# Kernel tuning notes

Measured on AMD Instinct MI355X. Metric: run time of the kernel, lower is better.

Reference implementation:

```python
import jax, jax.numpy as jnp
import numpy as np
import math

NUM_HEADS = 16  # power of two -> simple ALiBi slope formula

def alibi_slopes(num_heads: int) -> jnp.ndarray:
    # num_heads is a power of two here; general formula per Press et al. 2022
    k = 1 << (num_heads.bit_length() - 1)
    ratio = 2.0 ** (-8.0 / k)
    slopes = ratio ** np.arange(1, 1 + k)
    if num_heads != k:
        ratio2 = 2.0 ** (-8.0 / (2 * k))
        rest = (ratio2 ** np.arange(1, 1 + 2 * k, 2))[: num_heads - k]
        slopes = np.concatenate([slopes, rest])
    return jnp.asarray(slopes, dtype=jnp.float32).reshape(1, -1, 1, 1)


def setup_inputs() -> dict:
    key = jax.random.key(0)
    kq, kk, kv, km = jax.random.split(key, 4)
    B, H, S, D = 1, NUM_HEADS, 2048, 64
    query = jax.random.normal(kq, (B, H, S, D), dtype=jnp.float32)
    k_ = jax.random.normal(kk, (B, H, S, D), dtype=jnp.float32)
    value = jax.random.normal(kv, (B, H, S, D), dtype=jnp.float32)
    # padding-style boolean mask [B, S]; keep position 0 always valid
    mask = jax.random.randint(km, (B, S), 0, 2).astype(bool)
    mask = mask.at[:, 0].set(True)
    return {"query": query, "key": k_, "value": value, "mask": mask}


def reference(query, key, value, mask):
    B, H, S, D = query.shape
    scale = 1.0 / math.sqrt(D)
    # scores: [B, H, Sq, Sk]
    scores = jnp.einsum("bhqd,bhkd->bhqk", query, key) * scale
    # causal ALiBi bias: distances arange(1-S, 1) -> shape (1, H, 1, S)
    distances = jnp.arange(1 - S, 1, dtype=jnp.float32)
    bias = distances[None, None, None, :] * alibi_slopes(H)
    scores = scores + bias
    # boolean padding mask [B, S] -> [B, 1, 1, S]
    blocked = jnp.finfo(scores.dtype).min
    scores = jnp.where(mask[:, None, None, :], scores, blocked)
    weights = jax.nn.softmax(scores, axis=-1)
    # dropout_prob = 0.0 (eval) -> identity
    return jnp.einsum("bhqk,bhkd->bhqd", weights, value)
```

## Files before the change

kernel.cpp:

```cpp
#include <hip/hip_runtime.h>


constexpr int   S_LEN  = 2048;
constexpr int   D_DIM  = 64;
constexpr int   H_NUM  = 16;
constexpr int   QT     = 128;
constexpr int   K_TILE = 64;
constexpr int   NTILE  = S_LEN / K_TILE;
constexpr int   MAXNC  = 8;
constexpr int   QB     = S_LEN / QT;
constexpr int   HC0    = 6;
constexpr int   PROWSTR= 36;
constexpr float SCL    = 0.18033688f;
constexpr float L2E    = 1.44269504f;
constexpr float MASKED = -50000.0f;
constexpr float CUTOFF = 40.0f;

typedef short bf16x8 __attribute__((ext_vector_type(8)));
typedef short bf16x4 __attribute__((ext_vector_type(4)));
typedef float f32x4  __attribute__((ext_vector_type(4)));

__device__ inline short f2bf(float f) {
    union { float f; unsigned u; } x; x.f = f;
    return (short)((x.u + 0x7fffu + ((x.u >> 16) & 1u)) >> 16);
}

__device__ inline unsigned pack2bf(float a, float b) {
#if __has_builtin(__builtin_amdgcn_cvt_pk_bf16_f32)
    auto p = __builtin_amdgcn_cvt_pk_bf16_f32(a, b);
    unsigned u; __builtin_memcpy(&u, &p, 4); return u;
#else
    return (unsigned)(unsigned short)f2bf(a) | ((unsigned)(unsigned short)f2bf(b) << 16);
#endif
}

__device__ inline float fexp2(float x) {
#if __has_builtin(__builtin_amdgcn_exp2f)
    return __builtin_amdgcn_exp2f(x);
#else
    return exp2f(x);
#endif
}

__device__ inline unsigned permb(unsigned hi, unsigned lo, unsigned sel) {
#if __has_builtin(__builtin_amdgcn_perm)
    return __builtin_amdgcn_perm(hi, lo, sel);
#else
    return (sel == 0x05040100u) ? ((lo & 0xffffu) | (hi << 16))
                                : ((lo >> 16) | (hi & 0xffff0000u));
#endif
}

__device__ inline void load_lds16(const void* g, void* l) {
    __builtin_amdgcn_global_load_lds((const __attribute__((address_space(1))) void*)g,
                                     (__attribute__((address_space(3))) void*)l, 16, 0, 0);
}

__device__ inline int head_t0(int h) {
    const float slope_l2e = exp2f(-0.5f * (float)(h + 1)) * L2E;
    const float kmin = 2047.0f - CUTOFF / slope_l2e;
    return kmin <= 0.0f ? 0 : ((int)kmin) >> 6;
}
__device__ inline int head_nc(int h) {
    const int nt = NTILE - head_t0(h);
    const int nc = (nt + 3) >> 2;
    return nc > MAXNC ? MAXNC : nc;
}

__global__ __launch_bounds__(256)
void preprocess_kernel(const float* __restrict__ Qm, const float* __restrict__ Km,
                       const float* __restrict__ Vm, const void* __restrict__ maskp,
                       short* __restrict__ Qbf, short* __restrict__ Kswz,
                       short* __restrict__ Vswz, float* __restrict__ Bias)
{
    __shared__ int mask_is_i32;
    const int tid = threadIdx.x;
    const int kt = blockIdx.x, h = blockIdx.y;

    {
        const int row = kt * 64 + (tid >> 2);
        const int col = (tid & 3) << 4;
        const float* src = Qm + ((size_t)h * S_LEN + row) * D_DIM + col;
        short* dst = Qbf + ((size_t)h * S_LEN + row) * D_DIM + col;
        #pragma unroll
        for (int j = 0; j < 2; ++j) {
            float4 a = *(const float4*)(src + j * 8);
            float4 b = *(const float4*)(src + j * 8 + 4);
            unsigned u[4] = { pack2bf(a.x * SCL, a.y * SCL), pack2bf(a.z * SCL, a.w * SCL),
                              pack2bf(b.x * SCL, b.y * SCL), pack2bf(b.z * SCL, b.w * SCL) };
            bf16x8 qp; __builtin_memcpy(&qp, u, 16);
            *(bf16x8*)(dst + j * 8) = qp;
        }
    }

    if (kt < head_t0(h)) return;

    const int kbase = kt * K_TILE;
    const size_t tbase = ((size_t)h * S_LEN + kbase) * D_DIM;
    short* Kd = Kswz + ((size_t)h * NTILE + kt) * 4096;
    short* Vd = Vswz + ((size_t)h * NTILE + kt) * 4096;

    if (tid < 64) {
        const unsigned v = ((const unsigned*)maskp)[tid];
        const unsigned long long b = __ballot(v <= 1u);
        if (tid == 0) mask_is_i32 = (b == ~0ULL);
    }

    #pragma unroll
    for (int it = 0; it < 2; ++it) {
        const int idx = it * 256 + tid;
        const int key = idx >> 3, c = idx & 7;
        const float* src = Km + tbase + key * 64 + c * 8;
        float4 a = *(const float4*)src;
        float4 b = *(const float4*)(src + 4);
        unsigned u[4] = { pack2bf(a.x, a.y), pack2bf(a.z, a.w),
                          pack2bf(b.x, b.y), pack2bf(b.z, b.w) };
        bf16x8 kp; __builtin_memcpy(&kp, u, 16);
        *(bf16x8*)(Kd + key * 64 + ((c ^ (key & 7)) << 3)) = kp;
    }

    {
        const int db = tid >> 4, kb = tid & 15;
        const int d4 = db * 4, key4 = kb * 4;
        float4 vv[4];
        #pragma unroll
        for (int j = 0; j < 4; ++j)
            vv[j] = *(const float4*)(Vm + tbase + (key4 + j) * 64 + d4);
        const float* vp = (const float*)vv;
        #pragma unroll
        for (int jj = 0; jj < 4; ++jj) {
            const int d = d4 + jj;
            bf16x4 ov;
            ov[0] = f2bf(vp[0 * 4 + jj]); ov[1] = f2bf(vp[1 * 4 + jj]);
            ov[2] = f2bf(vp[2 * 4 + jj]); ov[3] = f2bf(vp[3 * 4 + jj]);
            *(bf16x4*)(Vd + d * 64 + (((key4 >> 3) ^ (d & 7)) << 3) + (key4 & 7)) = ov;
        }
    }
    __syncthreads();
    if (tid < K_TILE) {
        const int key = kbase + tid;
        const int mv = mask_is_i32 ? ((const int*)maskp)[key]
                                   : (int)((const unsigned char*)maskp)[key];
        const float slope_l2e = exp2f(-0.5f * (float)(h + 1)) * L2E;
        Bias[h * S_LEN + key] = mv ? slope_l2e * (float)(key - (S_LEN - 1)) : MASKED;
    }
}

__global__ __launch_bounds__(256, 4)
void attn_main(const short* __restrict__ Qbf, const short* __restrict__ Kswz,
               const short* __restrict__ Vswz, const float* __restrict__ Bias,
               float* __restrict__ Om, unsigned* __restrict__ Opart,
               float* __restrict__ lp)
{
    __shared__ short    k_lds[4096];
    __shared__ short    v_lds[4096];
    __shared__ float    bm_lds[64];
    __shared__ unsigned p_lds[4][32 * PROWSTR];

    const int tid = threadIdx.x;
    const int wave = tid >> 6, lane = tid & 63;
    const int l16 = lane & 15, quad = lane >> 4;
    const int h = blockIdx.y, qblk = blockIdx.x, c = blockIdx.z;

    const int nc = head_nc(h);
    if (c >= nc) return;
    const int t0 = head_t0(h);
    const int nt = NTILE - t0;
    const int tstart = t0 + (c * nt) / nc;
    const int tend   = t0 + ((c + 1) * nt) / nc;

    const unsigned psel = (quad < 2) ? 0x05040100u : 0x07060302u;

    bf16x8 qfrag[2][2];
    {
        const short* Qh = Qbf + (size_t)h * S_LEN * D_DIM;
        #pragma unroll
        for (int s = 0; s < 2; ++s) {
            const int qrow = qblk * QT + wave * 32 + s * 16 + l16;
            #pragma unroll
            for (int t = 0; t < 2; ++t)
                qfrag[s][t] = *(const bf16x8*)(Qh + (size_t)qrow * D_DIM + t * 32 + quad * 8);
        }
    }

    bf16x8 onesv;
    #pragma unroll
    for (int i = 0; i < 8; ++i) onesv[i] = (short)0x3F80;

    f32x4 o_frag[2][4], l4[2];
    #pragma unroll
    for (int s = 0; s < 2; ++s) {
        #pragma unroll
        for (int cc = 0; cc < 4; ++cc) o_frag[s][cc] = (f32x4){0.f, 0.f, 0.f, 0.f};
        l4[s] = (f32x4){0.f, 0.f, 0.f, 0.f};
    }

    const short* Kh = Kswz + (size_t)h * NTILE * 4096;
    const short* Vh = Vswz + (size_t)h * NTILE * 4096;
    const float* Bh = Bias + h * S_LEN;
    unsigned* pw = p_lds[wave];
    const int swz = l16 & 7;

    for (int kt = tstart; kt < tend; ++kt) {
        __syncthreads();
        {
            const char* kg = (const char*)(Kh + (size_t)kt * 4096);
            const char* vg = (const char*)(Vh + (size_t)kt * 4096);
            char* kl = (char*)k_lds + wave * 2048;
            char* vl = (char*)v_lds + wave * 2048;
            const int go = wave * 2048 + lane * 16;
            load_lds16(kg + go,        kl);
            load_lds16(kg + go + 1024, kl + 1024);
            load_lds16(vg + go,        vl);
            load_lds16(vg + go + 1024, vl + 1024);
        }
        if (tid < 16) {
            float4 b4 = *(const float4*)(Bh + kt * K_TILE + tid * 4);
            *(float4*)&bm_lds[tid * 4] = b4;
        }
        __syncthreads();

        f32x4 sv[2][4];
        #pragma unroll
        for (int cc = 0; cc < 4; ++cc) {
            const float b = bm_lds[cc * 16 + l16];
            const f32x4 binit = (f32x4){b, b, b, b};
            sv[0][cc] = binit;
            sv[1][cc] = binit;
            #pragma unroll
            for (int t = 0; t < 2; ++t) {
                bf16x8 bfrag = *(const bf16x8*)&k_lds[(cc * 16 + l16) * 64 + (((t * 4 + quad) ^ swz) << 3)];
                sv[0][cc] = __builtin_amdgcn_mfma_f32_16x16x32_bf16(qfrag[0][t], bfrag, sv[0][cc], 0, 0, 0);
                sv[1][cc] = __builtin_amdgcn_mfma_f32_16x16x32_bf16(qfrag[1][t], bfrag, sv[1][cc], 0, 0, 0);
            }
        }

        #pragma unroll
        for (int s = 0; s < 2; ++s) {
            #pragma unroll
            for (int r = 0; r < 4; ++r) {
                const float p0 = fexp2(sv[s][0][r]);
                const float p1 = fexp2(sv[s][1][r]);
                const float p2 = fexp2(sv[s][2][r]);
                const float p3 = fexp2(sv[s][3][r]);
                unsigned* pp = &pw[(s * 16 + quad * 4 + r) * PROWSTR + l16];
                pp[0]  = pack2bf(p0, p1);
                pp[16] = pack2bf(p2, p3);
            }
        }

        #pragma unroll
        for (int t2 = 0; t2 < 2; ++t2) {
            bf16x8 pfrag[2];
            #pragma unroll
            for (int s = 0; s < 2; ++s) {
                const unsigned* pr = &pw[(s * 16 + l16) * PROWSTR + t2 * 16 + (quad & 1) * 8];
                uint4 w0 = *(const uint4*)(pr);
                uint4 w1 = *(const uint4*)(pr + 4);
                unsigned pf[4];
                pf[0] = permb(w0.y, w0.x, psel);
                pf[1] = permb(w0.w, w0.z, psel);
                pf[2] = permb(w1.y, w1.x, psel);
                pf[3] = permb(w1.w, w1.z, psel);
                __builtin_memcpy(&pfrag[s], pf, 16);
            }
            #pragma unroll
            for (int c2 = 0; c2 < 4; ++c2) {
                bf16x8 vfrag = *(const bf16x8*)&v_lds[(c2 * 16 + l16) * 64 + (((t2 * 4 + quad) ^ swz) << 3)];
                o_frag[0][c2] = __builtin_amdgcn_mfma_f32_16x16x32_bf16(pfrag[0], vfrag, o_frag[0][c2], 0, 0, 0);
                o_frag[1][c2] = __builtin_amdgcn_mfma_f32_16x16x32_bf16(pfrag[1], vfrag, o_frag[1][c2], 0, 0, 0);
            }
            l4[0] = __builtin_amdgcn_mfma_f32_16x16x32_bf16(pfrag[0], onesv, l4[0], 0, 0, 0);
            l4[1] = __builtin_amdgcn_mfma_f32_16x16x32_bf16(pfrag[1], onesv, l4[1], 0, 0, 0);
        }
    }

    if (nc == 1) {
        float* Oh = Om + (size_t)h * S_LEN * D_DIM;
        const int qrow0 = qblk * QT + wave * 32;
        #pragma unroll
        for (int s = 0; s < 2; ++s) {
            #pragma unroll
            for (int r = 0; r < 4; ++r) {
                const float inv = 1.0f / l4[s][r];
                const int row = qrow0 + s * 16 + quad * 4 + r;
                float* dst = Oh + (size_t)row * D_DIM + l16;
                dst[0]  = o_frag[s][0][r] * inv;
                dst[16] = o_frag[s][1][r] * inv;
                dst[32] = o_frag[s][2][r] * inv;
                dst[48] = o_frag[s][3][r] * inv;
            }
        }
        return;
    }

    #pragma unroll
    for (int s = 0; s < 2; ++s) {
        const int g = qblk * 32 + wave * 8 + s * 4 + quad;
        const size_t gbase = (((size_t)h * MAXNC + c) * 512 + g);
        #pragma unroll
        for (int c2 = 0; c2 < 4; ++c2) {
            uint2 pk;
            pk.x = pack2bf(o_frag[s][c2][0], o_frag[s][c2][1]);
            pk.y = pack2bf(o_frag[s][c2][2], o_frag[s][c2][3]);
            *(uint2*)(Opart + (gbase * 64 + c2 * 16 + l16) * 2) = pk;
        }
        if (l16 == 0) *(f32x4*)(lp + gbase * 4) = l4[s];
    }
}

__global__ __launch_bounds__(256)
void attn_combine_kernel(const unsigned* __restrict__ Opart, const float* __restrict__ lp,
                         float* __restrict__ Om)
{
    const int t   = blockIdx.x * 256 + threadIdx.x;
    const int col = t & 63;
    const int g   = (t >> 6) & 511;
    const int h   = HC0 + (t >> 15);

    const int nc = head_nc(h);

    f32x4 den = (f32x4){0.f, 0.f, 0.f, 0.f};
    f32x4 acc = (f32x4){0.f, 0.f, 0.f, 0.f};
    for (int c = 0; c < nc; ++c) {
        const size_t gbase = (((size_t)h * MAXNC + c) * 512 + g);
        den += *(const f32x4*)(lp + gbase * 4);
        const uint2 pk = *(const uint2*)(Opart + (gbase * 64 + col) * 2);
        acc[0] += __int_as_float(pk.x << 16);
        acc[1] += __int_as_float((int)(pk.x & 0xffff0000u));
        acc[2] += __int_as_float(pk.y << 16);
        acc[3] += __int_as_float((int)(pk.y & 0xffff0000u));
    }
    float* Oh = Om + (size_t)h * S_LEN * D_DIM;
    #pragma unroll
    for (int r = 0; r < 4; ++r)
        Oh[(size_t)(g * 4 + r) * 64 + col] = acc[r] / den[r];
}

extern "C" void kernel_launch(void* const* d_in, const int* in_sizes, int n_in,
                              void* d_out, int out_size, void* d_ws, size_t ws_size,
                              hipStream_t stream) {
    (void)in_sizes; (void)n_in; (void)out_size; (void)ws_size;
    const float* Q = (const float*)d_in[0];
    const float* K = (const float*)d_in[1];
    const float* V = (const float*)d_in[2];
    const void*  M = d_in[3];
    float* O = (float*)d_out;

    char* ws = (char*)d_ws;
    size_t off = 0;
    short* Kswz = (short*)(ws + off); off += (size_t)H_NUM * S_LEN * D_DIM * 2;
    short* Vswz = (short*)(ws + off); off += (size_t)H_NUM * S_LEN * D_DIM * 2;
    short* Qbf  = (short*)(ws + off); off += (size_t)H_NUM * S_LEN * D_DIM * 2;
    float* Bias = (float*)(ws + off); off += (size_t)H_NUM * S_LEN * 4;
    unsigned* Opart = (unsigned*)(ws + off); off += (size_t)H_NUM * MAXNC * 512 * 64 * 8;
    float* lp   = (float*)(ws + off); off += (size_t)H_NUM * MAXNC * 512 * 4 * 4;

    preprocess_kernel<<<dim3(NTILE, H_NUM), 256, 0, stream>>>(Q, K, V, M, Qbf, Kswz, Vswz, Bias);
    attn_main<<<dim3(QB, H_NUM, MAXNC), 256, 0, stream>>>(Qbf, Kswz, Vswz, Bias, O, Opart, lp);
    attn_combine_kernel<<<((H_NUM - HC0) * 512 * 64) / 256, 256, 0, stream>>>(Opart, lp, O);
}
```

Measured before the change: 98.03 us.

## Double-buffer K/V/bias tiles in LDS to prefetch the next tile

Allocates two LDS buffers each for the K, V and bias tiles. The first tile is loaded before the main loop, and the next tile's global-to-LDS copy is issued at the top of each iteration while the current tile is computed. This hides load latency behind the MFMA work and cuts the barriers per iteration from two to one. In exchange LDS use per block grows, so the occupancy hint in launch bounds drops from 4 to 3 blocks per CU.

After: 100.0 us. 1.02x slower.

```diff
diff --git a/kernel.cpp b/kernel.cpp
--- a/kernel.cpp
+++ b/kernel.cpp
@@ -146,15 +146,15 @@
     }
 }
 
-__global__ __launch_bounds__(256, 4)
+__global__ __launch_bounds__(256, 3)
 void attn_main(const short* __restrict__ Qbf, const short* __restrict__ Kswz,
                const short* __restrict__ Vswz, const float* __restrict__ Bias,
                float* __restrict__ Om, unsigned* __restrict__ Opart,
                float* __restrict__ lp)
 {
-    __shared__ short    k_lds[4096];
-    __shared__ short    v_lds[4096];
-    __shared__ float    bm_lds[64];
+    __shared__ short    k_lds[2][4096];
+    __shared__ short    v_lds[2][4096];
+    __shared__ float    bm_lds[2][64];
     __shared__ unsigned p_lds[4][32 * PROWSTR];
 
     const int tid = threadIdx.x;
@@ -171,6 +171,26 @@
 
     const unsigned psel = (quad < 2) ? 0x05040100u : 0x07060302u;
 
+    const short* Kh = Kswz + (size_t)h * NTILE * 4096;
+    const short* Vh = Vswz + (size_t)h * NTILE * 4096;
+    const float* Bh = Bias + h * S_LEN;
+    const int go = wave * 2048 + lane * 16;
+
+    {
+        const char* kg = (const char*)(Kh + (size_t)tstart * 4096);
+        const char* vg = (const char*)(Vh + (size_t)tstart * 4096);
+        char* kl = (char*)k_lds[0] + wave * 2048;
+        char* vl = (char*)v_lds[0] + wave * 2048;
+        load_lds16(kg + go,        kl);
+        load_lds16(kg + go + 1024, kl + 1024);
+        load_lds16(vg + go,        vl);
+        load_lds16(vg + go + 1024, vl + 1024);
+        if (tid < 16) {
+            float4 b4 = *(const float4*)(Bh + tstart * K_TILE + tid * 4);
+            *(float4*)&bm_lds[0][tid * 4] = b4;
+        }
+    }
+
     bf16x8 qfrag[2][2];
     {
         const short* Qh = Qbf + (size_t)h * S_LEN * D_DIM;
@@ -195,41 +215,43 @@
         l4[s] = (f32x4){0.f, 0.f, 0.f, 0.f};
     }
 
-    const short* Kh = Kswz + (size_t)h * NTILE * 4096;
-    const short* Vh = Vswz + (size_t)h * NTILE * 4096;
-    const float* Bh = Bias + h * S_LEN;
     unsigned* pw = p_lds[wave];
     const int swz = l16 & 7;
 
+    __syncthreads();
+
     for (int kt = tstart; kt < tend; ++kt) {
-        __syncthreads();
-        {
-            const char* kg = (const char*)(Kh + (size_t)kt * 4096);
-            const char* vg = (const char*)(Vh + (size_t)kt * 4096);
-            char* kl = (char*)k_lds + wave * 2048;
-            char* vl = (char*)v_lds + wave * 2048;
-            const int go = wave * 2048 + lane * 16;
+        const int buf = (kt - tstart) & 1;
+
+        if (kt + 1 < tend) {
+            const char* kg = (const char*)(Kh + (size_t)(kt + 1) * 4096);
+            const char* vg = (const char*)(Vh + (size_t)(kt + 1) * 4096);
+            char* kl = (char*)k_lds[buf ^ 1] + wave * 2048;
+            char* vl = (char*)v_lds[buf ^ 1] + wave * 2048;
             load_lds16(kg + go,        kl);
             load_lds16(kg + go + 1024, kl + 1024);
             load_lds16(vg + go,        vl);
             load_lds16(vg + go + 1024, vl + 1024);
-        }
-        if (tid < 16) {
-            float4 b4 = *(const float4*)(Bh + kt * K_TILE + tid * 4);
-            *(float4*)&bm_lds[tid * 4] = b4;
-        }
-        __syncthreads();
+            if (tid < 16) {
+                float4 b4 = *(const float4*)(Bh + (kt + 1) * K_TILE + tid * 4);
+                *(float4*)&bm_lds[buf ^ 1][tid * 4] = b4;
+            }
+        }
+
+        const short* kb = k_lds[buf];
+        const short* vb = v_lds[buf];
+        const float* bm = bm_lds[buf];
 
         f32x4 sv[2][4];
         #pragma unroll
         for (int cc = 0; cc < 4; ++cc) {
-            const float b = bm_lds[cc * 16 + l16];
+            const float b = bm[cc * 16 + l16];
             const f32x4 binit = (f32x4){b, b, b, b};
             sv[0][cc] = binit;
             sv[1][cc] = binit;
             #pragma unroll
             for (int t = 0; t < 2; ++t) {
-                bf16x8 bfrag = *(const bf16x8*)&k_lds[(cc * 16 + l16) * 64 + (((t * 4 + quad) ^ swz) << 3)];
+                bf16x8 bfrag = *(const bf16x8*)&kb[(cc * 16 + l16) * 64 + (((t * 4 + quad) ^ swz) << 3)];
                 sv[0][cc] = __builtin_amdgcn_mfma_f32_16x16x32_bf16(qfrag[0][t], bfrag, sv[0][cc], 0, 0, 0);
                 sv[1][cc] = __builtin_amdgcn_mfma_f32_16x16x32_bf16(qfrag[1][t], bfrag, sv[1][cc], 0, 0, 0);
             }
@@ -266,13 +288,15 @@
             }
             #pragma unroll
             for (int c2 = 0; c2 < 4; ++c2) {
-                bf16x8 vfrag = *(const bf16x8*)&v_lds[(c2 * 16 + l16) * 64 + (((t2 * 4 + quad) ^ swz) << 3)];
+                bf16x8 vfrag = *(const bf16x8*)&vb[(c2 * 16 + l16) * 64 + (((t2 * 4 + quad) ^ swz) << 3)];
                 o_frag[0][c2] = __builtin_amdgcn_mfma_f32_16x16x32_bf16(pfrag[0], vfrag, o_frag[0][c2], 0, 0, 0);
                 o_frag[1][c2] = __builtin_amdgcn_mfma_f32_16x16x32_bf16(pfrag[1], vfrag, o_frag[1][c2], 0, 0, 0);
             }
             l4[0] = __builtin_amdgcn_mfma_f32_16x16x32_bf16(pfrag[0], onesv, l4[0], 0, 0, 0);
             l4[1] = __builtin_amdgcn_mfma_f32_16x16x32_bf16(pfrag[1], onesv, l4[1], 0, 0, 0);
         }
+
+        __syncthreads();
     }
 
     if (nc == 1) {
```
